# Optimization experiments

Measured on AMD Instinct MI355X. Metric: run time of the kernel, lower is better.

The kernel has to match this reference:

```python
import jax, jax.numpy as jnp
import numpy as np


def setup_inputs() -> dict:
    key = jax.random.key(0)
    k1, k2 = jax.random.split(key)
    B, N, S = 25, 16, 5  # batch MUST be 25 (== S*S) for the original's broadcast to be legal
    pred = jax.random.normal(k1, (B, S * S * 3), dtype=jnp.float32)
    truth = jax.random.randint(k2, (B, N, 2), 0, 66, dtype=jnp.int64)
    return {"pred": pred, "truth": truth, "S": S}


def reference(pred, truth, S):
    B = pred.shape[0]
    N = truth.shape[1]
    C = S * S
    truth = truth.astype(jnp.float32)

    prediction = pred.reshape(B, C, 3)
    conf = prediction[:, :, 0]          # (B, C)
    coord = prediction[:, :, 1:3]       # (B, C, 2)

    cell = 80.0 / S                      # 16.0
    tx = (truth[:, :, 0] + 14.0) % cell * (S / 80.0)   # (B, N) in [0,1)
    ty = (truth[:, :, 1] + 14.0) % cell * (S / 80.0)
    label = (jnp.floor((truth[:, :, 0] + 14.0) / cell) * S
             + jnp.floor((truth[:, :, 1] + 14.0) / cell)).astype(jnp.int32)  # (B, N)

    # --- p_loss: emulate the original's overwrite semantics ---
    # Loop 2 overwrites cell j with 0.5*conf^2 whenever ANY object has label != j.
    # Hence the IOU term from loop 1 survives only in cells where ALL objects map,
    # and the surviving write is from the LAST object (x = N-1).
    counts = jax.nn.one_hot(label, C, dtype=jnp.float32).sum(axis=1)  # (B, C)
    all_match = counts == N

    tx_last = tx[:, -1:]  # (B, 1)
    ty_last = ty[:, -1:]
    dx = jnp.abs(coord[:, :, 0] * 16.0 - tx_last * 16.0)  # (B, C)
    dy = jnp.abs(coord[:, :, 1] * 16.0 - ty_last * 16.0)
    iou = (jnp.maximum(28.0 - 2.0 * dx, 0.0) * jnp.maximum(28.0 - 2.0 * dy, 0.0)) \
          / ((28.0 + dx) * (28.0 + dy))

    p_loss = jnp.where(all_match, (conf - iou) ** 2, 0.5 * conf ** 2)[:, :, None]  # (B, C, 1)

    # --- dis_loss: indexed by OBJECT index j (not cell), padded to C ---
    px = jnp.take_along_axis(coord[:, :, 0], label, axis=1)  # (B, N)
    py = jnp.take_along_axis(coord[:, :, 1], label, axis=1)
    d = (px - tx) ** 2 + (py - ty) ** 2                      # (B, N)
    dis_loss = jnp.zeros((B, C), jnp.float32).at[:, :N].set(5.0 * d)

    # Original broadcast: (B, C) + (B, C, 1) -> (C, B, C) [valid since B == C]
    loss1 = jnp.mean(dis_loss + p_loss, axis=1)  # (C, C)... actually (B, C) after mean
    loss2 = jnp.mean(loss1, axis=0)              # (C,)
    return loss2
```

## Files before the change

kernel.cpp:

```cpp
#include <hip/hip_runtime.h>


#define NT 256

__global__ __launch_bounds__(NT) void loss_26405458936156_kernel(
    const float* __restrict__ pred,
    const int*   __restrict__ truth,
    float*       __restrict__ out,
    int B)
{
    const float cell  = 16.0f;
    const float cellr = 0.0625f;

    __shared__ float s_pred[64 * 75];
    __shared__ int   s_lab[64][17];
    __shared__ float s_dis[64][17];
    __shared__ float s_txl[64], s_tyl[64];

    const int t = threadIdx.x;

    const int PN = B * 75;
    for (int i = t; i < PN; i += NT) s_pred[i] = pred[i];

    const int2* tr = (const int2*)truth;
    for (int i = t; i < B * 16; i += NT) {
        int b = i >> 4, n = i & 15;
        int2 tv = tr[i];
        float t0 = (float)tv.x + 14.0f;
        float t1 = (float)tv.y + 14.0f;
        float fx = floorf(t0 * cellr);
        float fy = floorf(t1 * cellr);
        float tx = (t0 - fx * cell) * cellr;
        float ty = (t1 - fy * cell) * cellr;
        int   lb = (int)fx * 5 + (int)fy;
        s_lab[b][n] = lb;
        if (n == 15) { s_txl[b] = tx * 16.0f; s_tyl[b] = ty * 16.0f; }
        float px = pred[b * 75 + 3 * lb + 1];
        float py = pred[b * 75 + 3 * lb + 2];
        float ex = px - tx, ey = py - ty;
        s_dis[b][n] = 5.0f * (ex * ex + ey * ey);
    }
    __syncthreads();

    if (t < 64) {
        int   amc = -1;
        float txl = 0.0f, tyl = 0.0f;
        if (t < B) {
            int l0 = s_lab[t][0], all = 1;
            #pragma unroll
            for (int n = 1; n < 16; ++n) all &= (s_lab[t][n] == l0);
            amc = all ? l0 : -1;
            txl = s_txl[t];
            tyl = s_tyl[t];
        }

        float psum = 0.0f;
        for (int i = t; i < B * 25; i += 64) {
            int b = i / 25, c = i - b * 25;
            const float* pc = &s_pred[b * 75 + 3 * c];
            float conf = pc[0], cx = pc[1], cy = pc[2];
            int   amcb = __shfl(amc, b);
            float txlb = __shfl(txl, b);
            float tylb = __shfl(tyl, b);
            float dx = fabsf(cx * 16.0f - txlb);
            float dy = fabsf(cy * 16.0f - tylb);
            float iou = fmaxf(28.0f - 2.0f * dx, 0.0f) * fmaxf(28.0f - 2.0f * dy, 0.0f)
                      / ((28.0f + dx) * (28.0f + dy));
            float e = conf - iou;
            psum += (amcb == c) ? e * e : 0.5f * conf * conf;
        }
        #pragma unroll
        for (int o = 32; o; o >>= 1) psum += __shfl_xor(psum, o);

        if (t < 25) {
            float P = psum * (1.0f / (float)(B * 25));
            float acc = 0.0f;
            if (t < 16) {
                for (int b = 0; b < B; ++b) acc += s_dis[b][t];
                acc *= 1.0f / (float)B;
            }
            out[t] = acc + P;
        }
    }
}

extern "C" void kernel_launch(void* const* d_in, const int* in_sizes, int n_in,
                              void* d_out, int out_size, void* d_ws, size_t ws_size,
                              hipStream_t stream) {
    const float* pred  = (const float*)d_in[0];
    const int*   truth = (const int*)d_in[1];
    float*       out   = (float*)d_out;

    const int B = in_sizes[0] / 75;

    loss_26405458936156_kernel<<<1, NT, 0, stream>>>(pred, truth, out, B);
}
```

Baseline: 9.463 us.

## Spread p_loss across all four wavefronts and vectorize input loads

The truth loads are issued up front, before the pred copy, so their latency overlaps. Pred is copied into shared memory with float4 loads. The p_loss loop now runs on all 256 threads instead of one wavefront. Per-wave partial sums are combined through shared memory after a second barrier. This trades an extra __syncthreads for less serial work in the single-block kernel, and it assumes B <= 32 and B*16 <= 512.

Result: slower. 16.46 us (+74.0%).

```diff
diff --git a/kernel.cpp b/kernel.cpp
--- a/kernel.cpp
+++ b/kernel.cpp
@@ -12,20 +12,37 @@
     const float cell  = 16.0f;
     const float cellr = 0.0625f;
 
-    __shared__ float s_pred[64 * 75];
-    __shared__ int   s_lab[64][17];
-    __shared__ float s_dis[64][17];
-    __shared__ float s_txl[64], s_tyl[64];
+    __shared__ float4 s_pred4[480];
+    __shared__ int    s_lab[32][17];
+    __shared__ float  s_dis[32][17];
+    __shared__ float  s_txl[32], s_tyl[32];
+    __shared__ float  s_wsum[4];
+    float* s_pred = (float*)s_pred4;
 
-    const int t = threadIdx.x;
+    const int t    = threadIdx.x;
+    const int lane = t & 63;
+
+    const int2* tr = (const int2*)truth;
+    const int   TN = B * 16;
+    int2 tv0, tv1;
+    const bool h0 = t < TN;
+    const bool h1 = t + NT < TN;
+    if (h0) tv0 = tr[t];
+    if (h1) tv1 = tr[t + NT];
 
     const int PN = B * 75;
-    for (int i = t; i < PN; i += NT) s_pred[i] = pred[i];
+    const int n4 = PN >> 2;
+    const float4* pr4 = (const float4*)pred;
+    for (int s = t; s < n4; s += NT) s_pred4[s] = pr4[s];
+    if (t < PN - (n4 << 2)) s_pred[(n4 << 2) + t] = pred[(n4 << 2) + t];
 
-    const int2* tr = (const int2*)truth;
-    for (int i = t; i < B * 16; i += NT) {
+    #pragma unroll
+    for (int u = 0; u < 2; ++u) {
+        const bool h = u ? h1 : h0;
+        if (!h) continue;
+        const int  i  = u ? t + NT : t;
+        const int2 tv = u ? tv1 : tv0;
         int b = i >> 4, n = i & 15;
-        int2 tv = tr[i];
         float t0 = (float)tv.x + 14.0f;
         float t1 = (float)tv.y + 14.0f;
         float fx = floorf(t0 * cellr);
@@ -42,45 +59,46 @@
     }
     __syncthreads();
 
-    if (t < 64) {
-        int   amc = -1;
-        float txl = 0.0f, tyl = 0.0f;
-        if (t < B) {
-            int l0 = s_lab[t][0], all = 1;
-            #pragma unroll
-            for (int n = 1; n < 16; ++n) all &= (s_lab[t][n] == l0);
-            amc = all ? l0 : -1;
-            txl = s_txl[t];
-            tyl = s_tyl[t];
+    int   amc = -1;
+    float txl = 0.0f, tyl = 0.0f;
+    if (lane < B) {
+        int l0 = s_lab[lane][0], all = 1;
+        #pragma unroll
+        for (int n = 1; n < 16; ++n) all &= (s_lab[lane][n] == l0);
+        amc = all ? l0 : -1;
+        txl = s_txl[lane];
+        tyl = s_tyl[lane];
+    }
+
+    float psum = 0.0f;
+    for (int i = t; i < B * 25; i += NT) {
+        int b = i / 25, c = i - b * 25;
+        const float* pc = &s_pred[b * 75 + 3 * c];
+        float conf = pc[0], cx = pc[1], cy = pc[2];
+        int   amcb = __shfl(amc, b);
+        float txlb = __shfl(txl, b);
+        float tylb = __shfl(tyl, b);
+        float dx = fabsf(cx * 16.0f - txlb);
+        float dy = fabsf(cy * 16.0f - tylb);
+        float iou = fmaxf(28.0f - 2.0f * dx, 0.0f) * fmaxf(28.0f - 2.0f * dy, 0.0f)
+                  / ((28.0f + dx) * (28.0f + dy));
+        float e = conf - iou;
+        psum += (amcb == c) ? e * e : 0.5f * conf * conf;
+    }
+    #pragma unroll
+    for (int o = 32; o; o >>= 1) psum += __shfl_xor(psum, o);
+    if (lane == 0) s_wsum[t >> 6] = psum;
+    __syncthreads();
+
+    if (t < 25) {
+        float P = (s_wsum[0] + s_wsum[1] + s_wsum[2] + s_wsum[3])
+                  * (1.0f / (float)(B * 25));
+        float acc = 0.0f;
+        if (t < 16) {
+            for (int b = 0; b < B; ++b) acc += s_dis[b][t];
+            acc *= 1.0f / (float)B;
         }
-
-        float psum = 0.0f;
-        for (int i = t; i < B * 25; i += 64) {
-            int b = i / 25, c = i - b * 25;
-            const float* pc = &s_pred[b * 75 + 3 * c];
-            float conf = pc[0], cx = pc[1], cy = pc[2];
-            int   amcb = __shfl(amc, b);
-            float txlb = __shfl(txl, b);
-            float tylb = __shfl(tyl, b);
-            float dx = fabsf(cx * 16.0f - txlb);
-            float dy = fabsf(cy * 16.0f - tylb);
-            float iou = fmaxf(28.0f - 2.0f * dx, 0.0f) * fmaxf(28.0f - 2.0f * dy, 0.0f)
-                      / ((28.0f + dx) * (28.0f + dy));
-            float e = conf - iou;
-            psum += (amcb == c) ? e * e : 0.5f * conf * conf;
-        }
-        #pragma unroll
-        for (int o = 32; o; o >>= 1) psum += __shfl_xor(psum, o);
-
-        if (t < 25) {
-            float P = psum * (1.0f / (float)(B * 25));
-            float acc = 0.0f;
-            if (t < 16) {
-                for (int b = 0; b < B; ++b) acc += s_dis[b][t];
-                acc *= 1.0f / (float)B;
-            }
-            out[t] = acc + P;
-        }
+        out[t] = acc + P;
     }
 }
 
```
